# Kernel tuning notes

Hardware: AMD Instinct MI355X
Metric: run time of the kernel (lower is better)

Reference implementation:

```python
import jax, jax.numpy as jnp
import numpy as np

EPS = 1e-12  # F.normalize default eps

def _l2norm(x):
    return x / jnp.maximum(jnp.linalg.norm(x, axis=-1, keepdims=True), EPS)

def setup_inputs() -> dict:
    key = jax.random.key(0)
    k1, k2, k3 = jax.random.split(key, 3)
    N, C, D = 131072, 1000, 256
    feat = jax.random.normal(k1, (N, D), dtype=jnp.float32)
    # memory bank is initialized to L2-normalized centers in the original (init())
    memory = _l2norm(jax.random.normal(k2, (C, D), dtype=jnp.float32))
    label = jax.random.randint(k3, (N,), 0, C, dtype=jnp.int64)
    return {"feat": feat, "memory": memory, "label": label}

def reference(feat, memory, label):
    num_cls, feat_dim = memory.shape
    N = feat.shape[0]
    t = 1.0  # forward default temperature

    featn = _l2norm(feat)

    # --- update(feat, label): fused per-class masked gather+sum as one segment_sum ---
    f = jax.lax.stop_gradient(featn)  # feat.detach() in original
    sums = jax.ops.segment_sum(f, label, num_segments=num_cls)          # [C, D]
    counts = jax.ops.segment_sum(jnp.ones((N,), f.dtype), label, num_segments=num_cls)
    flags = (counts > 0).astype(f.dtype)[:, None]                        # [C, 1]
    batch_center = _l2norm(sums) * flags                                 # zeros for empty classes

    # --- update_center_by_simi ---
    simi = jnp.sum(memory * batch_center, axis=-1, keepdims=True)        # [C, 1]
    update_wei = 1.0 - (1.0 - simi) * flags                              # [C, 1]
    new_memory = _l2norm(update_wei * memory + (1.0 - update_wei) * batch_center)

    # --- similarity + cross entropy ---
    simis = jnp.einsum('nd,cd->nc', featn, new_memory) / t               # [N, C]
    logp = jax.nn.log_softmax(simis, axis=-1)
    loss = -jnp.mean(jnp.take_along_axis(logp, label[:, None], axis=1))
    return loss
```

## Files before the change

### kernel.cpp

```cpp
#include <hip/hip_runtime.h>
#include <hip/hip_fp8.h>

#define NROWS 131072
#define NCLS  1000
#define CPAD  1024
#define DDIM  256

typedef __attribute__((ext_vector_type(4))) float f32x4;
typedef __attribute__((ext_vector_type(2))) long l64x2;

__device__ __forceinline__ float wred(float v){
#pragma unroll
  for (int m = 1; m < 64; m <<= 1) v += __shfl_xor(v, m, 64);
  return v;
}

__device__ __forceinline__ float fexp2(float x){
#if __has_builtin(__builtin_amdgcn_exp2f)
  return __builtin_amdgcn_exp2f(x);
#else
  float r; asm("v_exp_f32 %0, %1" : "=v"(r) : "v"(x)); return r;
#endif
}

__device__ __forceinline__ unsigned pk4_fp8(float a, float b, float c, float d){
#if __has_builtin(__builtin_amdgcn_cvt_pk_fp8_f32)
  int v = __builtin_amdgcn_cvt_pk_fp8_f32(a, b, 0, false);
  v = __builtin_amdgcn_cvt_pk_fp8_f32(c, d, v, true);
  return (unsigned)v;
#else
  __hip_fp8_e4m3 fa(a), fb(b), fc(c), fd(d);
  return (unsigned)fa.__x | ((unsigned)fb.__x<<8) |
         ((unsigned)fc.__x<<16) | ((unsigned)fd.__x<<24);
#endif
}

__device__ __forceinline__ void store_frag8(unsigned char* nmem, int c, int ln,
                                            float a, float b, float x, float y){
  int ch = c >> 5, nb = (c >> 4) & 1, r16 = c & 15;
  int k = ln >> 3, g = (ln >> 1) & 3, q = ln & 1;
  *(unsigned*)(nmem + ch*8192 + k*1024 + (g*16+r16)*16 + nb*8 + q*4) =
      pk4_fp8(a, b, x, y);
}

__global__ __launch_bounds__(1024) void k_center(
    const float* __restrict__ feat, const float* __restrict__ memory,
    const int* __restrict__ label, unsigned char* __restrict__ nmem,
    float* __restrict__ nmemf32){
  const int c0 = blockIdx.x * 2;
  const int t = threadIdx.x;
  const int w = t >> 6, lane = t & 63;
  if (c0 >= NCLS){
    if (t < 128) store_frag8(nmem, c0 + (t >> 6), t & 63, 0.f, 0.f, 0.f, 0.f);
    return;
  }
  const int c1 = c0 + 1;
  __shared__ float4 accred[2][16][64];
  __shared__ int cw[2][16];

  float4 a0 = make_float4(0.f,0.f,0.f,0.f);
  float4 a1 = make_float4(0.f,0.f,0.f,0.f);
  int cnt0 = 0, cnt1 = 0;
  const float4* feat4 = (const float4*)feat;
  const int4*   lab4  = (const int4*)label;

  for (int it = 0; it < 32; ++it){
    int base = (w*32 + it) * 256;
    int4 lv = lab4[base/4 + lane];
#pragma unroll
    for (int sub = 0; sub < 4; ++sub){
      int lvv = (sub==0)?lv.x:(sub==1)?lv.y:(sub==2)?lv.z:lv.w;
      unsigned long long m0 = __ballot(lvv == c0);
      unsigned long long m1 = __ballot(lvv == c1);
      cnt0 += (int)__popcll(m0); cnt1 += (int)__popcll(m1);
      while (m0){
        int b = __ffsll((long long)m0) - 1; m0 &= m0 - 1;
        int r = base + b*4 + sub;
        float4 x = feat4[r*64 + lane];
        float ss = wred(x.x*x.x + x.y*x.y + x.z*x.z + x.w*x.w);
        float sc = 1.0f / fmaxf(sqrtf(ss), 1e-12f);
        a0.x += x.x*sc; a0.y += x.y*sc; a0.z += x.z*sc; a0.w += x.w*sc;
      }
      while (m1){
        int b = __ffsll((long long)m1) - 1; m1 &= m1 - 1;
        int r = base + b*4 + sub;
        float4 x = feat4[r*64 + lane];
        float ss = wred(x.x*x.x + x.y*x.y + x.z*x.z + x.w*x.w);
        float sc = 1.0f / fmaxf(sqrtf(ss), 1e-12f);
        a1.x += x.x*sc; a1.y += x.y*sc; a1.z += x.z*sc; a1.w += x.w*sc;
      }
    }
  }
  accred[0][w][lane] = a0; accred[1][w][lane] = a1;
  if (lane == 0){ cw[0][w] = cnt0; cw[1][w] = cnt1; }
  __syncthreads();

  if (t < 128){
    int cls = t >> 6, ln = t & 63;
    float sx=0.f, sy=0.f, sz=0.f, sw=0.f; int total = 0;
#pragma unroll
    for (int s = 0; s < 16; ++s){
      float4 v = accred[cls][s][ln];
      sx += v.x; sy += v.y; sz += v.z; sw += v.w;
      total += cw[cls][s];
    }
    int c = c0 + cls;
    float ss = wred(sx*sx + sy*sy + sz*sz + sw*sw);
    float inv = 1.0f / fmaxf(sqrtf(ss), 1e-12f);
    float bx = sx*inv, by = sy*inv, bz = sz*inv, bw = sw*inv;
    float flag = (total > 0) ? 1.0f : 0.0f;
    float4 m = ((const float4*)memory)[c*64 + ln];
    float simi = wred(m.x*bx + m.y*by + m.z*bz + m.w*bw);
    float wei = 1.0f - (1.0f - simi)*flag;
    float rx = wei*m.x + (1.0f-wei)*bx;
    float ry = wei*m.y + (1.0f-wei)*by;
    float rz = wei*m.z + (1.0f-wei)*bz;
    float rw = wei*m.w + (1.0f-wei)*bw;
    float ss2 = wred(rx*rx + ry*ry + rz*rz + rw*rw);
    float inv2 = 1.0f / fmaxf(sqrtf(ss2), 1e-12f);
    store_frag8(nmem, c, ln, rx*inv2, ry*inv2, rz*inv2, rw*inv2);
    ((float4*)nmemf32)[c*64 + ln] =
        make_float4(rx*inv2, ry*inv2, rz*inv2, rw*inv2);
  }
}

#define MFMA8 __builtin_amdgcn_mfma_f32_16x16x32_fp8_fp8

__global__ __launch_bounds__(256, 2) void k_gemm(
    const float* __restrict__ feat, const unsigned char* __restrict__ nmem,
    const float* __restrict__ nmemf32, const int* __restrict__ label,
    float* __restrict__ partials){
  __shared__ float bred[4];
  const int t = threadIdx.x, w = t >> 6, lane = t & 63;
  const int g = lane >> 4, r16 = lane & 15;
  const int rowbase = blockIdx.x * 128;

  long areg[2][8];
  float slabv[2];
#pragma unroll
  for (int mf = 0; mf < 2; ++mf){
    int row = rowbase + w*32 + mf*16 + r16;
    const float4* rp = (const float4*)(feat + row*DDIM);
    float ss = 0.f;
#pragma unroll
    for (int kt = 0; kt < 8; ++kt){
      float4 x0 = rp[kt*8 + g*2];
      float4 x1 = rp[kt*8 + g*2 + 1];
      ss += x0.x*x0.x + x0.y*x0.y + x0.z*x0.z + x0.w*x0.w
          + x1.x*x1.x + x1.y*x1.y + x1.z*x1.z + x1.w*x1.w;
    }
    ss += __shfl_xor(ss, 16, 64);
    ss += __shfl_xor(ss, 32, 64);
    float invn = 1.0f / fmaxf(sqrtf(ss), 1e-12f);
    float sc = 1.44269504f * invn;
    int lab = label[row];
    const float4* bp4 = (const float4*)(nmemf32 + (size_t)lab*DDIM);
    float dl = 0.f;
#pragma unroll
    for (int kt = 0; kt < 8; ++kt){
      float4 x0 = rp[kt*8 + g*2];
      float4 x1 = rp[kt*8 + g*2 + 1];
      float4 b0 = bp4[kt*8 + g*2];
      float4 b1 = bp4[kt*8 + g*2 + 1];
      unsigned lo = pk4_fp8(x0.x*sc, x0.y*sc, x0.z*sc, x0.w*sc);
      unsigned hi = pk4_fp8(x1.x*sc, x1.y*sc, x1.z*sc, x1.w*sc);
      areg[mf][kt] = (long)(((unsigned long)hi << 32) | lo);
      dl += x0.x*b0.x + x0.y*b0.y + x0.z*b0.z + x0.w*b0.w
          + x1.x*b1.x + x1.y*b1.y + x1.z*b1.z + x1.w*b1.w;
    }
    dl += __shfl_xor(dl, 16, 64);
    dl += __shfl_xor(dl, 32, 64);
    slabv[mf] = dl * invn;
  }
  float slab_epi[2][4];
#pragma unroll
  for (int m = 0; m < 2; ++m)
#pragma unroll
    for (int j = 0; j < 4; ++j)
      slab_epi[m][j] = __shfl(slabv[m], g*4 + j, 16);

  float esum[2][4] = {{0.f,0.f,0.f,0.f},{0.f,0.f,0.f,0.f}};

  const char* nbp = (const char*)nmem + lane*16;
  const int rot = blockIdx.x & 31;
  long bA[8], bB[8];

#define LOADLO(CH)                                                            \
  { const char* cb = nbp + (size_t)(CH)*8192;                                 \
    _Pragma("unroll")                                                         \
    for (int k2 = 0; k2 < 4; ++k2){                                           \
      l64x2 v = *(const l64x2*)(cb + k2*1024);                                \
      bA[k2*2] = v.x; bA[k2*2+1] = v.y; } }
#define LOADHI(CH)                                                            \
  { const char* cb = nbp + (size_t)(CH)*8192 + 4096;                          \
    _Pragma("unroll")                                                         \
    for (int k2 = 0; k2 < 4; ++k2){                                           \
      l64x2 v = *(const l64x2*)(cb + k2*1024);                                \
      bB[k2*2] = v.x; bB[k2*2+1] = v.y; } }

  LOADLO(rot); LOADHI(rot);

  for (int it = 0; it < 32; ++it){
    int nxt = (it + 1 + rot) & 31;

    f32x4 acc[2][2];
    __builtin_amdgcn_s_setprio(1);
    {
      f32x4 Z = {0.f,0.f,0.f,0.f};
      acc[0][0] = MFMA8(areg[0][0], bA[0], Z, 0, 0, 0);
      acc[0][1] = MFMA8(areg[0][0], bA[1], Z, 0, 0, 0);
      acc[1][0] = MFMA8(areg[1][0], bA[0], Z, 0, 0, 0);
      acc[1][1] = MFMA8(areg[1][0], bA[1], Z, 0, 0, 0);
    }
#pragma unroll
    for (int k = 1; k < 4; ++k){
      acc[0][0] = MFMA8(areg[0][k], bA[k*2+0], acc[0][0], 0, 0, 0);
      acc[0][1] = MFMA8(areg[0][k], bA[k*2+1], acc[0][1], 0, 0, 0);
      acc[1][0] = MFMA8(areg[1][k], bA[k*2+0], acc[1][0], 0, 0, 0);
      acc[1][1] = MFMA8(areg[1][k], bA[k*2+1], acc[1][1], 0, 0, 0);
    }
    __builtin_amdgcn_s_setprio(0);

    if (it < 31) LOADLO(nxt);

    __builtin_amdgcn_s_setprio(1);
#pragma unroll
    for (int k = 4; k < 8; ++k){
      acc[0][0] = MFMA8(areg[0][k], bB[(k-4)*2+0], acc[0][0], 0, 0, 0);
      acc[0][1] = MFMA8(areg[0][k], bB[(k-4)*2+1], acc[0][1], 0, 0, 0);
      acc[1][0] = MFMA8(areg[1][k], bB[(k-4)*2+0], acc[1][0], 0, 0, 0);
      acc[1][1] = MFMA8(areg[1][k], bB[(k-4)*2+1], acc[1][1], 0, 0, 0);
    }
    __builtin_amdgcn_s_setprio(0);

    if (it < 31) LOADHI(nxt);

#pragma unroll
    for (int m = 0; m < 2; ++m)
#pragma unroll
      for (int n = 0; n < 2; ++n)
#pragma unroll
        for (int j = 0; j < 4; ++j)
          esum[m][j] += fexp2(acc[m][n][j]);
  }

  float v = 0.f;
#pragma unroll
  for (int m = 0; m < 2; ++m)
#pragma unroll
    for (int j = 0; j < 4; ++j){
      float e = esum[m][j];
      e += __shfl_xor(e, 1, 64); e += __shfl_xor(e, 2, 64);
      e += __shfl_xor(e, 4, 64); e += __shfl_xor(e, 8, 64);
      v += 0.69314718056f * __log2f(e - 24.0f) - slab_epi[m][j];
    }
  if (r16 != 0) v = 0.f;
  v = wred(v);
  if (lane == 0) bred[w] = v;
  __syncthreads();
  if (t == 0) partials[blockIdx.x] = bred[0] + bred[1] + bred[2] + bred[3];
}

__global__ __launch_bounds__(256) void k_final(
    const float* __restrict__ partials, float* __restrict__ out){
  const int t = threadIdx.x;
  const int w = t >> 6, lane = t & 63;
  __shared__ float red[4];
  float s = partials[t] + partials[t+256] + partials[t+512] + partials[t+768];
  s = wred(s);
  if (lane == 0) red[w] = s;
  __syncthreads();
  if (t == 0) out[0] = (red[0]+red[1]+red[2]+red[3]) * (1.0f/(float)NROWS);
}

extern "C" void kernel_launch(void* const* d_in, const int* in_sizes, int n_in,
                              void* d_out, int out_size, void* d_ws, size_t ws_size,
                              hipStream_t stream){
  const float* feat   = (const float*)d_in[0];
  const float* memory = (const float*)d_in[1];
  const int*   label  = (const int*)d_in[2];
  float* out = (float*)d_out;
  unsigned char* nmem = (unsigned char*)d_ws;
  float* nmemf32 = (float*)((char*)d_ws + 262144);
  float* partials = (float*)((char*)d_ws + 1310720);

  k_center<<<CPAD/2, 1024, 0, stream>>>(feat, memory, label, nmem, nmemf32);
  k_gemm<<<NROWS/128, 256, 0, stream>>>(feat, nmem, nmemf32, label, partials);
  k_final<<<1, 256, 0, stream>>>(partials, out);
}
```

Measured before the change: 112.3 us.

## Restructure B-fragment layout into 16-class chunks with triple-buffered prefetch

Changes the packed fp8 memory layout from 32-class chunks (split into lo/hi k halves) to 16-class chunks holding the full K dimension. The main loop now iterates over 64 chunks with a 3-deep register ring buffer, prefetching two chunks ahead instead of splitting one chunk's load across its two MFMA halves. This is meant to hide load latency better and shorten the dependency chains per iteration, at the cost of more live registers and more loop iterations with smaller MFMA batches.

```diff
diff --git a/kernel.cpp b/kernel.cpp
--- a/kernel.cpp
+++ b/kernel.cpp
@@ -37,9 +37,9 @@
 
 __device__ __forceinline__ void store_frag8(unsigned char* nmem, int c, int ln,
                                             float a, float b, float x, float y){
-  int ch = c >> 5, nb = (c >> 4) & 1, r16 = c & 15;
+  int c2 = c >> 4, r16c = c & 15;
   int k = ln >> 3, g = (ln >> 1) & 3, q = ln & 1;
-  *(unsigned*)(nmem + ch*8192 + k*1024 + (g*16+r16)*16 + nb*8 + q*4) =
+  *(unsigned*)(nmem + c2*4096 + (k>>1)*1024 + (g*16+r16c)*16 + (k&1)*8 + q*4) =
       pk4_fp8(a, b, x, y);
 }
 
@@ -182,67 +182,47 @@
   float esum[2][4] = {{0.f,0.f,0.f,0.f},{0.f,0.f,0.f,0.f}};
 
   const char* nbp = (const char*)nmem + lane*16;
-  const int rot = blockIdx.x & 31;
-  long bA[8], bB[8];
-
-#define LOADLO(CH)                                                            \
-  { const char* cb = nbp + (size_t)(CH)*8192;                                 \
+  const int rot = blockIdx.x & 63;
+  long b0[8], b1[8], b2[8];
+
+#define LOADC(BUF, C)                                                         \
+  { const char* cb = nbp + (size_t)(((C) + rot) & 63)*4096;                   \
     _Pragma("unroll")                                                         \
     for (int k2 = 0; k2 < 4; ++k2){                                           \
       l64x2 v = *(const l64x2*)(cb + k2*1024);                                \
-      bA[k2*2] = v.x; bA[k2*2+1] = v.y; } }
-#define LOADHI(CH)                                                            \
-  { const char* cb = nbp + (size_t)(CH)*8192 + 4096;                          \
+      BUF[k2*2] = v.x; BUF[k2*2+1] = v.y; } }
+
+#define BODY(CUR, PF, CIDX)                                                   \
+  {                                                                           \
+    if ((CIDX) + 2 < 64) LOADC(PF, (CIDX)+2);           \
+    f32x4 a0_, a1_;                                                           \
+    __builtin_amdgcn_s_setprio(1);                                            \
+    { f32x4 Z = {0.f,0.f,0.f,0.f};                                            \
+      a0_ = MFMA8(areg[0][0], CUR[0], Z, 0, 0, 0);                            \
+      a1_ = MFMA8(areg[1][0], CUR[0], Z, 0, 0, 0); }                          \
     _Pragma("unroll")                                                         \
-    for (int k2 = 0; k2 < 4; ++k2){                                           \
-      l64x2 v = *(const l64x2*)(cb + k2*1024);                                \
-      bB[k2*2] = v.x; bB[k2*2+1] = v.y; } }
-
-  LOADLO(rot); LOADHI(rot);
-
-  for (int it = 0; it < 32; ++it){
-    int nxt = (it + 1 + rot) & 31;
-
-    f32x4 acc[2][2];
-    __builtin_amdgcn_s_setprio(1);
-    {
-      f32x4 Z = {0.f,0.f,0.f,0.f};
-      acc[0][0] = MFMA8(areg[0][0], bA[0], Z, 0, 0, 0);
-      acc[0][1] = MFMA8(areg[0][0], bA[1], Z, 0, 0, 0);
-      acc[1][0] = MFMA8(areg[1][0], bA[0], Z, 0, 0, 0);
-      acc[1][1] = MFMA8(areg[1][0], bA[1], Z, 0, 0, 0);
-    }
-#pragma unroll
-    for (int k = 1; k < 4; ++k){
-      acc[0][0] = MFMA8(areg[0][k], bA[k*2+0], acc[0][0], 0, 0, 0);
-      acc[0][1] = MFMA8(areg[0][k], bA[k*2+1], acc[0][1], 0, 0, 0);
-      acc[1][0] = MFMA8(areg[1][k], bA[k*2+0], acc[1][0], 0, 0, 0);
-      acc[1][1] = MFMA8(areg[1][k], bA[k*2+1], acc[1][1], 0, 0, 0);
-    }
-    __builtin_amdgcn_s_setprio(0);
-
-    if (it < 31) LOADLO(nxt);
-
-    __builtin_amdgcn_s_setprio(1);
-#pragma unroll
-    for (int k = 4; k < 8; ++k){
-      acc[0][0] = MFMA8(areg[0][k], bB[(k-4)*2+0], acc[0][0], 0, 0, 0);
-      acc[0][1] = MFMA8(areg[0][k], bB[(k-4)*2+1], acc[0][1], 0, 0, 0);
-      acc[1][0] = MFMA8(areg[1][k], bB[(k-4)*2+0], acc[1][0], 0, 0, 0);
-      acc[1][1] = MFMA8(areg[1][k], bB[(k-4)*2+1], acc[1][1], 0, 0, 0);
-    }
-    __builtin_amdgcn_s_setprio(0);
-
-    if (it < 31) LOADHI(nxt);
-
-#pragma unroll
-    for (int m = 0; m < 2; ++m)
-#pragma unroll
-      for (int n = 0; n < 2; ++n)
-#pragma unroll
-        for (int j = 0; j < 4; ++j)
-          esum[m][j] += fexp2(acc[m][n][j]);
-  }
+    for (int k = 1; k < 8; ++k){                                              \
+      a0_ = MFMA8(areg[0][k], CUR[k], a0_, 0, 0, 0);                          \
+      a1_ = MFMA8(areg[1][k], CUR[k], a1_, 0, 0, 0);                          \
+    }                                                                         \
+    __builtin_amdgcn_s_setprio(0);                                            \
+    _Pragma("unroll")                                                         \
+    for (int j = 0; j < 4; ++j){                                              \
+      esum[0][j] += fexp2(a0_[j]);                                            \
+      esum[1][j] += fexp2(a1_[j]);                                            \
+    }                                                                         \
+  }
+
+  LOADC(b0, 0);
+  LOADC(b1, 1);
+
+  for (int p = 0; p < 21; ++p){
+    int c = 3*p;
+    BODY(b0, b2, c);
+    BODY(b1, b0, c+1);
+    BODY(b2, b1, c+2);
+  }
+  BODY(b0, b1, 63);
 
   float v = 0.f;
 #pragma unroll
```

Measured after the change: 113.4 us. About the same (+1.0%).
